# Kernel tuning notes

Hardware: AMD Instinct MI355X
Metric: run time of the kernel (lower is better)

## Reference

```python
import jax, jax.numpy as jnp
import numpy as np

B, T_IN, D = 16, 512, 256
MAX_DUR = 16


def setup_inputs() -> dict:
    key = jax.random.key(0)
    k1, k2 = jax.random.split(key)
    duration = jax.random.randint(k1, (B, T_IN), 0, MAX_DUR, dtype=jnp.int32)
    encoder_outputs = jax.random.normal(k2, (B, T_IN, D), dtype=jnp.float32)
    mask = jnp.ones((B, T_IN), dtype=bool)
    return {"encoder_outputs": encoder_outputs, "duration": duration, "mask": mask}


def reference(encoder_outputs, duration, mask):
    # duration is a concrete int array here, so T_out is a static Python int
    t_max = int(jnp.max(jnp.sum(duration, axis=-1)))
    d = duration.astype(jnp.float32)
    # frame centers per token: c[b, i] = cumsum(d)[b, i] - 0.5 * d[b, i]
    c = (jnp.cumsum(d, axis=-1) - 0.5 * d)[:, :, None]          # [B, T_in, 1]
    t = jnp.arange(1, t_max + 1, dtype=jnp.float32)[None, None, :]  # [1, 1, T_out]
    w1 = jnp.exp(-0.1 * (t - c) ** 2)                           # [B, T_in, T_out]
    w2 = jnp.sum(w1, axis=1, keepdims=True)                     # [B, 1, T_out]
    w2 = jnp.where(w2 == 0.0, 1.0, w2)
    w = w1 / w2                                                 # [B, T_in, T_out]
    # out[b, t, d] = sum_i w[b, i, t] * enc[b, i, d]
    out = jnp.einsum('bit,bid->btd', w, encoder_outputs)        # [B, T_out, D]
    return (out, w)
```

## Files before the change

### kernel.cpp

```cpp
#include <hip/hip_runtime.h>

#define B_    16
#define T_IN  512
#define D_    256
#define TM    128
#define KI    32
#define AP    40
#define BP    40

typedef __attribute__((ext_vector_type(8))) short short8;
typedef __attribute__((ext_vector_type(4))) float f32x4;

__device__ __forceinline__ unsigned short f2bf(float x) {
    unsigned u = __builtin_bit_cast(unsigned, x);
    u += 0x7fff + ((u >> 16) & 1);
    return (unsigned short)(u >> 16);
}

__global__ __launch_bounds__(256, 2) void fused_kernel(
    const float* __restrict__ enc,
    const int*   __restrict__ dur,
    float* __restrict__ out,
    float* __restrict__ wout,
    int t_out)
{
    __shared__ int   sd[T_IN];
    __shared__ float sc[T_IN];
    __shared__ float sinv[TM];
    __shared__ float red[TM];
    __shared__ __align__(16) unsigned short A_lds[TM * AP];
    __shared__ __align__(16) unsigned short B_lds[D_ * BP];

    const int tid = threadIdx.x;
    const int b   = blockIdx.y;
    const int t0  = blockIdx.x * TM;

    const int v0 = dur[b * T_IN + tid];
    const int v1 = dur[b * T_IN + tid + 256];
    sd[tid] = v0;
    sd[tid + 256] = v1;
    __syncthreads();
    for (int off = 1; off < T_IN; off <<= 1) {
        const int a0 = (tid >= off) ? sd[tid - off] : 0;
        const int a1 = sd[tid + 256 - off];
        __syncthreads();
        sd[tid] += a0;
        sd[tid + 256] += a1;
        __syncthreads();
    }
    sc[tid]       = (float)sd[tid]       - 0.5f * (float)v0;
    sc[tid + 256] = (float)sd[tid + 256] - 0.5f * (float)v1;
    __syncthreads();

    const int tl   = tid & 127;
    const int half = tid >> 7;
    const float tv = (float)(t0 + tl + 1);
    {
        float s = 0.f;
        const int i0 = half * 256;
        for (int i = 0; i < 256; ++i) {
            const float d = tv - sc[i0 + i];
            s += __expf(-0.1f * d * d);
        }
        if (half == 0) red[tl] = s;
        __syncthreads();
        if (half == 1) red[tl] += s;
        __syncthreads();
        if (half == 0) {
            const float w2 = red[tl];
            sinv[tl] = (w2 == 0.f) ? 1.f : 1.f / w2;
        }
        __syncthreads();
    }

    if (t0 + tl < t_out) {
        const float inv = sinv[tl];
        const int i0 = half * 256;
        float* wp = wout + ((long long)b * T_IN + i0) * t_out + (t0 + tl);
        for (int i = 0; i < 256; ++i) {
            const float d = tv - sc[i0 + i];
            wp[(long long)i * t_out] = __expf(-0.1f * d * d) * inv;
        }
    }

    const int lane = tid & 63;
    const int wave = tid >> 6;
    const int wm   = wave & 1;
    const int wn   = wave >> 1;
    const int mrow = lane & 15;
    const int quad = lane >> 4;

    f32x4 acc[4][8];
    #pragma unroll
    for (int mf = 0; mf < 4; ++mf)
        #pragma unroll
        for (int nf = 0; nf < 8; ++nf)
            acc[mf][nf] = (f32x4){0.f, 0.f, 0.f, 0.f};

    for (int kc = 0; kc < T_IN; kc += KI) {
        __syncthreads();

        {
            const int t_loc = tid & 127;
            const int i0    = (tid >> 7) * 16;
            const float tvs = (float)(t0 + t_loc + 1);
            unsigned short tmp[16];
            #pragma unroll
            for (int j = 0; j < 16; ++j) {
                const float d = tvs - sc[kc + i0 + j];
                tmp[j] = f2bf(__expf(-0.1f * d * d));
            }
            *(short8*)&A_lds[t_loc * AP + i0]     = *(const short8*)&tmp[0];
            *(short8*)&A_lds[t_loc * AP + i0 + 8] = *(const short8*)&tmp[8];
        }
        {
            const int dq = (lane) * 4;
            #pragma unroll
            for (int p = 0; p < 8; ++p) {
                const int il = wave + p * 4;
                const float4 ev = *(const float4*)&enc[((long long)b * T_IN + kc + il) * D_ + dq];
                B_lds[(dq + 0) * BP + il] = f2bf(ev.x);
                B_lds[(dq + 1) * BP + il] = f2bf(ev.y);
                B_lds[(dq + 2) * BP + il] = f2bf(ev.z);
                B_lds[(dq + 3) * BP + il] = f2bf(ev.w);
            }
        }
        __syncthreads();

        short8 av[4];
        #pragma unroll
        for (int mf = 0; mf < 4; ++mf)
            av[mf] = *(const short8*)&A_lds[(wm * 64 + mf * 16 + mrow) * AP + quad * 8];
        #pragma unroll
        for (int nf = 0; nf < 8; ++nf) {
            const short8 bv = *(const short8*)&B_lds[(wn * 128 + nf * 16 + mrow) * BP + quad * 8];
            #pragma unroll
            for (int mf = 0; mf < 4; ++mf)
                acc[mf][nf] = __builtin_amdgcn_mfma_f32_16x16x32_bf16(av[mf], bv, acc[mf][nf], 0, 0, 0);
        }
    }

    #pragma unroll
    for (int mf = 0; mf < 4; ++mf) {
        #pragma unroll
        for (int r = 0; r < 4; ++r) {
            const int tloc = wm * 64 + mf * 16 + quad * 4 + r;
            const int t = t0 + tloc;
            if (t < t_out) {
                const float inv = sinv[tloc];
                #pragma unroll
                for (int nf = 0; nf < 8; ++nf) {
                    const int d = wn * 128 + nf * 16 + mrow;
                    out[((long long)b * t_out + t) * D_ + d] = acc[mf][nf][r] * inv;
                }
            }
        }
    }
}

extern "C" void kernel_launch(void* const* d_in, const int* in_sizes, int n_in,
                              void* d_out, int out_size, void* d_ws, size_t ws_size,
                              hipStream_t stream) {
    const float* enc = (const float*)d_in[0];
    const int*   dur = (const int*)d_in[1];

    const int t_out = out_size / (B_ * (D_ + T_IN));

    float* out  = (float*)d_out;
    float* wout = (float*)d_out + (size_t)B_ * t_out * D_;

    dim3 grid((t_out + TM - 1) / TM, B_);
    fused_kernel<<<grid, 256, 0, stream>>>(enc, dur, out, wout, t_out);
}
```

Baseline: 291.3 us.

## Halve time tile, fuse weight write into GEMM loop, load encoder operands directly

Result: faster. 260.9 us (-10.4%).

```diff
diff --git a/kernel.cpp b/kernel.cpp
--- a/kernel.cpp
+++ b/kernel.cpp
@@ -3,10 +3,9 @@
 #define B_    16
 #define T_IN  512
 #define D_    256
-#define TM    128
+#define TM    64
 #define KI    32
 #define AP    40
-#define BP    40
 
 typedef __attribute__((ext_vector_type(8))) short short8;
 typedef __attribute__((ext_vector_type(4))) float f32x4;
@@ -17,7 +16,7 @@
     return (unsigned short)(u >> 16);
 }
 
-__global__ __launch_bounds__(256, 2) void fused_kernel(
+__global__ __launch_bounds__(256, 3) void fused_kernel(
     const float* __restrict__ enc,
     const int*   __restrict__ dur,
     float* __restrict__ out,
@@ -26,10 +25,9 @@
 {
     __shared__ int   sd[T_IN];
     __shared__ float sc[T_IN];
+    __shared__ float red[4][TM];
     __shared__ float sinv[TM];
-    __shared__ float red[TM];
     __shared__ __align__(16) unsigned short A_lds[TM * AP];
-    __shared__ __align__(16) unsigned short B_lds[D_ * BP];
 
     const int tid = threadIdx.x;
     const int b   = blockIdx.y;
@@ -52,88 +50,73 @@
     sc[tid + 256] = (float)sd[tid + 256] - 0.5f * (float)v1;
     __syncthreads();
 
-    const int tl   = tid & 127;
-    const int half = tid >> 7;
-    const float tv = (float)(t0 + tl + 1);
+    const int tq = tid & 63;
+    const int qq = tid >> 6;
+    const float tv = (float)(t0 + tq + 1);
+
     {
         float s = 0.f;
-        const int i0 = half * 256;
-        for (int i = 0; i < 256; ++i) {
+        const int i0 = qq * 128;
+        for (int i = 0; i < 128; ++i) {
             const float d = tv - sc[i0 + i];
             s += __expf(-0.1f * d * d);
         }
-        if (half == 0) red[tl] = s;
+        red[qq][tq] = s;
         __syncthreads();
-        if (half == 1) red[tl] += s;
-        __syncthreads();
-        if (half == 0) {
-            const float w2 = red[tl];
-            sinv[tl] = (w2 == 0.f) ? 1.f : 1.f / w2;
+        if (qq == 0) {
+            const float w2 = red[0][tq] + red[1][tq] + red[2][tq] + red[3][tq];
+            sinv[tq] = (w2 == 0.f) ? 1.f : 1.f / w2;
         }
         __syncthreads();
     }
+    const float inv_t = sinv[tq];
+    const bool  t_ok  = (t0 + tq) < t_out;
 
-    if (t0 + tl < t_out) {
-        const float inv = sinv[tl];
-        const int i0 = half * 256;
-        float* wp = wout + ((long long)b * T_IN + i0) * t_out + (t0 + tl);
-        for (int i = 0; i < 256; ++i) {
-            const float d = tv - sc[i0 + i];
-            wp[(long long)i * t_out] = __expf(-0.1f * d * d) * inv;
-        }
-    }
+    const int lane  = tid & 63;
+    const int wave  = tid >> 6;
+    const int mrow  = lane & 15;
+    const int quad  = lane >> 4;
+    const int dbase = wave * 64;
+    const int iq0   = qq * 8;
 
-    const int lane = tid & 63;
-    const int wave = tid >> 6;
-    const int wm   = wave & 1;
-    const int wn   = wave >> 1;
-    const int mrow = lane & 15;
-    const int quad = lane >> 4;
-
-    f32x4 acc[4][8];
+    f32x4 acc[4][4];
     #pragma unroll
     for (int mf = 0; mf < 4; ++mf)
         #pragma unroll
-        for (int nf = 0; nf < 8; ++nf)
+        for (int nf = 0; nf < 4; ++nf)
             acc[mf][nf] = (f32x4){0.f, 0.f, 0.f, 0.f};
+
+    const float* encB = enc + (long long)b * T_IN * D_;
+    float* wB = wout + (long long)b * T_IN * t_out + (t0 + tq);
 
     for (int kc = 0; kc < T_IN; kc += KI) {
         __syncthreads();
 
         {
-            const int t_loc = tid & 127;
-            const int i0    = (tid >> 7) * 16;
-            const float tvs = (float)(t0 + t_loc + 1);
-            unsigned short tmp[16];
+            unsigned short tmp[8];
             #pragma unroll
-            for (int j = 0; j < 16; ++j) {
-                const float d = tvs - sc[kc + i0 + j];
-                tmp[j] = f2bf(__expf(-0.1f * d * d));
+            for (int j = 0; j < 8; ++j) {
+                const float d = tv - sc[kc + iq0 + j];
+                const float e = __expf(-0.1f * d * d);
+                tmp[j] = f2bf(e);
+                if (t_ok) wB[(long long)(kc + iq0 + j) * t_out] = e * inv_t;
             }
-            *(short8*)&A_lds[t_loc * AP + i0]     = *(const short8*)&tmp[0];
-            *(short8*)&A_lds[t_loc * AP + i0 + 8] = *(const short8*)&tmp[8];
-        }
-        {
-            const int dq = (lane) * 4;
-            #pragma unroll
-            for (int p = 0; p < 8; ++p) {
-                const int il = wave + p * 4;
-                const float4 ev = *(const float4*)&enc[((long long)b * T_IN + kc + il) * D_ + dq];
-                B_lds[(dq + 0) * BP + il] = f2bf(ev.x);
-                B_lds[(dq + 1) * BP + il] = f2bf(ev.y);
-                B_lds[(dq + 2) * BP + il] = f2bf(ev.z);
-                B_lds[(dq + 3) * BP + il] = f2bf(ev.w);
-            }
+            *(short8*)&A_lds[tq * AP + iq0] = *(const short8*)tmp;
         }
         __syncthreads();
 
         short8 av[4];
         #pragma unroll
         for (int mf = 0; mf < 4; ++mf)
-            av[mf] = *(const short8*)&A_lds[(wm * 64 + mf * 16 + mrow) * AP + quad * 8];
+            av[mf] = *(const short8*)&A_lds[(mf * 16 + mrow) * AP + quad * 8];
+
         #pragma unroll
-        for (int nf = 0; nf < 8; ++nf) {
-            const short8 bv = *(const short8*)&B_lds[(wn * 128 + nf * 16 + mrow) * BP + quad * 8];
+        for (int nf = 0; nf < 4; ++nf) {
+            const float* p = encB + (long long)(kc + quad * 8) * D_ + dbase + nf * 16 + mrow;
+            unsigned short bt[8];
+            #pragma unroll
+            for (int j = 0; j < 8; ++j) bt[j] = f2bf(p[j * D_]);
+            const short8 bv = *(const short8*)bt;
             #pragma unroll
             for (int mf = 0; mf < 4; ++mf)
                 acc[mf][nf] = __builtin_amdgcn_mfma_f32_16x16x32_bf16(av[mf], bv, acc[mf][nf], 0, 0, 0);
@@ -144,15 +127,13 @@
     for (int mf = 0; mf < 4; ++mf) {
         #pragma unroll
         for (int r = 0; r < 4; ++r) {
-            const int tloc = wm * 64 + mf * 16 + quad * 4 + r;
-            const int t = t0 + tloc;
+            const int tl = mf * 16 + quad * 4 + r;
+            const int t  = t0 + tl;
             if (t < t_out) {
-                const float inv = sinv[tloc];
+                const float inv = sinv[tl];
                 #pragma unroll
-                for (int nf = 0; nf < 8; ++nf) {
-                    const int d = wn * 128 + nf * 16 + mrow;
-                    out[((long long)b * t_out + t) * D_ + d] = acc[mf][nf][r] * inv;
-                }
+                for (int nf = 0; nf < 4; ++nf)
+                    out[((long long)b * t_out + t) * D_ + dbase + nf * 16 + mrow] = acc[mf][nf][r] * inv;
             }
         }
     }
```
